# Performance work log

Hardware: AMD Instinct MI355X
Metric: run time of the kernel (lower is better)

The kernel has to match this reference:

```python
import jax, jax.numpy as jnp
import numpy as np

RADIUS = 400.0
FIELD = 8000.0  # um extent of slide coordinate field


def setup_inputs() -> dict:
    key = jax.random.key(0)
    ks = jax.random.split(key, 8)
    B, N, D, H, K = 4, 4096, 1536, 512, 8
    images = jax.random.normal(ks[0], (B, N, D), dtype=jnp.float32)
    positions = jax.random.uniform(ks[1], (B, N, 2), dtype=jnp.float32) * FIELD
    W_feat = jax.random.normal(ks[2], (D, H), dtype=jnp.float32) * (1.0 / np.sqrt(D))
    b_feat = jnp.zeros((H,), dtype=jnp.float32)
    W_pos = jax.random.normal(ks[3], (2, H), dtype=jnp.float32) * 0.5
    W_gnn = jax.random.normal(ks[4], (H, H), dtype=jnp.float32) * (1.0 / np.sqrt(H))
    W_self = jax.random.normal(ks[5], (H, H), dtype=jnp.float32) * (1.0 / np.sqrt(H))
    anchors = jax.random.normal(ks[6], (K, D), dtype=jnp.float32)
    return {"images": images, "positions": positions, "W_feat": W_feat,
            "b_feat": b_feat, "W_pos": W_pos, "W_gnn": W_gnn,
            "W_self": W_self, "anchors": anchors}


def _radius_adjacency(pos):
    # pos: (N, 2). Dense O(N^2) radius graph (mirrors torch.cdist + mask).
    sq = jnp.sum(pos * pos, axis=-1)                       # (N,)
    d2 = sq[:, None] + sq[None, :] - 2.0 * (pos @ pos.T)   # (N, N)
    mask = d2 < (RADIUS * RADIUS)
    N = pos.shape[0]
    mask = mask & ~jnp.eye(N, dtype=bool)                  # no self-loops
    return mask.astype(pos.dtype)


def reference(images, positions, W_feat, b_feat, W_pos, W_gnn, W_self, anchors):
    # --- Stream A: explicit concept quantifier (cosine sim to anchors) ---
    x_norm = images / jnp.clip(jnp.linalg.norm(images, axis=-1, keepdims=True), 1e-12)
    a_norm = anchors / jnp.clip(jnp.linalg.norm(anchors, axis=-1, keepdims=True), 1e-12)
    scores = jnp.einsum('bnd,kd->bnk', x_norm, a_norm)     # (B, N, K)
    concept_profile = scores.mean(axis=1)                  # (B, K)

    # --- Stream B: feature extraction with positional encoding ---
    feat = images @ W_feat + b_feat + positions @ W_pos    # (B, N, H)

    # --- radius graph + one mean-aggregation GNN layer, per slide ---
    def per_graph(f, p):
        A = _radius_adjacency(p)                           # (N, N)
        deg = jnp.clip(A.sum(axis=-1, keepdims=True), 1.0) # (N, 1)
        h = jax.nn.relu(f)
        agg = (A @ h) / deg                                # mean over neighbors
        return jax.nn.relu(agg @ W_gnn + f @ W_self)       # (N, H)

    refined = jax.vmap(per_graph)(feat, positions)         # (B, N, H)
    latent_spatial = refined.mean(axis=1)                  # (B, H)  per-graph mean pool

    return jnp.concatenate([latent_spatial, concept_profile], axis=1)  # (B, H+K)
```

## Files before the change

kernel.cpp:

```cpp
#include <hip/hip_runtime.h>

#define B_ 4
#define N_ 4096
#define D_ 1536
#define H_ 512
#define K_ 8
#define M_ (B_*N_)
#define R2_ 160000.0f
#define CAP 192

typedef __attribute__((ext_vector_type(8))) short bf16x8;
typedef __attribute__((ext_vector_type(4))) float f32x4;

__device__ __forceinline__ unsigned short f2bf(float f) {
  union { float f; unsigned u; } v; v.f = f;
  unsigned r = (v.u + 0x7FFFu + ((v.u >> 16) & 1u)) >> 16;
  return (unsigned short)r;
}

typedef const __attribute__((address_space(1))) unsigned int gas_u32;
typedef __attribute__((address_space(3))) unsigned int las_u32;
__device__ __forceinline__ void gl_lds16(const unsigned short* g, unsigned short* l) {
  __builtin_amdgcn_global_load_lds((gas_u32*)g, (las_u32*)l, 16, 0, 0);
}

__global__ __launch_bounds__(256) void k_prep(
    const float* __restrict__ Wf, const float* __restrict__ Wg, const float* __restrict__ Ws,
    const float* __restrict__ anchors, unsigned short* __restrict__ WfT,
    unsigned short* __restrict__ WgsT, float* __restrict__ anorm) {
  __shared__ float t[64][65];
  __shared__ float red[4];
  int bx = blockIdx.x, by = blockIdx.y, tid = threadIdx.x;
  if (by == 40) {
    int k = bx;
    float s = 0.f;
    for (int i = tid; i < D_; i += 256) { float v = anchors[k*D_ + i]; s += v*v; }
    #pragma unroll
    for (int off = 32; off; off >>= 1) s += __shfl_down(s, off);
    if ((tid & 63) == 0) red[tid >> 6] = s;
    __syncthreads();
    if (tid == 0) anorm[k] = fmaxf(sqrtf(red[0]+red[1]+red[2]+red[3]), 1e-12f);
    return;
  }
  const float* W; unsigned short* WT; int kt, outStride, outOff;
  if (by < 24)      { W = Wf; WT = WfT;  kt = by;      outStride = D_;   outOff = 0; }
  else if (by < 32) { W = Wg; WT = WgsT; kt = by - 24; outStride = 1024; outOff = 0; }
  else              { W = Ws; WT = WgsT; kt = by - 32; outStride = 1024; outOff = 512; }
  int tx = tid & 63, ty = tid >> 6;
  #pragma unroll
  for (int r = 0; r < 64; r += 4)
    t[ty + r][tx] = W[(size_t)(kt*64 + ty + r)*H_ + bx*64 + tx];
  __syncthreads();
  #pragma unroll
  for (int r = 0; r < 64; r += 4) {
    int n = bx*64 + ty + r;
    WT[(size_t)n*outStride + outOff + kt*64 + tx] = f2bf(t[tx][ty + r]);
  }
}

__global__ __launch_bounds__(256) void k_concept_cast(
    const float* __restrict__ images, const float* __restrict__ anchors,
    const float* __restrict__ anorm, unsigned short* __restrict__ imgs_bf,
    float* __restrict__ out) {
  __shared__ float sA[K_*D_];
  __shared__ float sc[4][K_];
  int tid = threadIdx.x, lane = tid & 63, w = tid >> 6;
  {
    const float4* a4 = (const float4*)anchors;
    float4* sA4 = (float4*)sA;
    #pragma unroll
    for (int i = 0; i < 12; i++) sA4[tid + 256*i] = a4[tid + 256*i];
  }
  __syncthreads();
  float acc_k[K_] = {};
  for (int r = 0; r < 8; r++) {
    int gm = blockIdx.x*32 + w*8 + r;
    const float4* xrow = (const float4*)(images + (size_t)gm*D_);
    float nrm = 0.f; float dot[K_] = {};
    #pragma unroll
    for (int it = 0; it < 6; it++) {
      int j = lane + 64*it;
      float4 x = xrow[j];
      nrm += x.x*x.x + x.y*x.y + x.z*x.z + x.w*x.w;
      #pragma unroll
      for (int k = 0; k < K_; k++) {
        float4 a = *(const float4*)&sA[(size_t)(k*384 + j)*4];
        dot[k] += x.x*a.x + x.y*a.y + x.z*a.z + x.w*a.w;
      }
      ushort4 s;
      s.x = f2bf(x.x); s.y = f2bf(x.y); s.z = f2bf(x.z); s.w = f2bf(x.w);
      *(ushort4*)&imgs_bf[(size_t)gm*D_ + (size_t)j*4] = s;
    }
    #pragma unroll
    for (int off = 32; off; off >>= 1) {
      nrm += __shfl_down(nrm, off);
      #pragma unroll
      for (int k = 0; k < K_; k++) dot[k] += __shfl_down(dot[k], off);
    }
    if (lane == 0) {
      float inv = 1.0f / fmaxf(sqrtf(nrm), 1e-12f);
      #pragma unroll
      for (int k = 0; k < K_; k++) acc_k[k] += dot[k] * inv / anorm[k];
    }
  }
  if (lane == 0) {
    #pragma unroll
    for (int k = 0; k < K_; k++) sc[w][k] = acc_k[k];
  }
  __syncthreads();
  if (tid < K_) {
    float s = sc[0][tid] + sc[1][tid] + sc[2][tid] + sc[3][tid];
    int b = blockIdx.x >> 7;
    atomicAdd(out + b*(H_+K_) + H_ + tid, s * (1.0f/N_));
  }
}

#define BM 128
#define BN 128
#define BK 32

__global__ __launch_bounds__(256) void k_gemm(
    const unsigned short* __restrict__ A, const unsigned short* __restrict__ BT,
    int Kdim, int mode, const float* __restrict__ bias, const float* __restrict__ Wpos,
    const float* __restrict__ positions, unsigned short* __restrict__ AB,
    float* __restrict__ out) {
  __shared__ unsigned short As[BM*BK];
  __shared__ unsigned short Bs[BN*BK];
  __shared__ float colsum[BN];
  int tid = threadIdx.x;
  int lane = tid & 63, wv = tid >> 6;
  int wm = wv >> 1, wn = wv & 1;
  int l15 = lane & 15, quad = lane >> 4;
  int bx = blockIdx.x;
  int bm = bx >> 2, bn = bx & 3;
  int m0 = bm*BM, n0 = bn*BN;

  f32x4 acc[4][4] = {};

  int c = wv*2;
  int rowc = (lane >> 2), seg = lane & 3;
  const unsigned short* gA0 = A  + (size_t)(m0 + c*16 + rowc)*Kdim + seg*8;
  const unsigned short* gA1 = gA0 + (size_t)16*Kdim;
  const unsigned short* gB0 = BT + (size_t)(n0 + c*16 + rowc)*Kdim + seg*8;
  const unsigned short* gB1 = gB0 + (size_t)16*Kdim;
  unsigned short* lA0 = As + c*512;
  unsigned short* lA1 = lA0 + 512;
  unsigned short* lB0 = Bs + c*512;
  unsigned short* lB1 = lB0 + 512;

  int nk = Kdim / BK;
  for (int kt = 0; kt < nk; kt++) {
    __syncthreads();
    gl_lds16(gA0, lA0); gl_lds16(gA1, lA1);
    gl_lds16(gB0, lB0); gl_lds16(gB1, lB1);
    gA0 += BK; gA1 += BK; gB0 += BK; gB1 += BK;
    __syncthreads();

    bf16x8 aF[4], bF[4];
    #pragma unroll
    for (int f = 0; f < 4; f++)
      aF[f] = *(const bf16x8*)&As[(wm*64 + f*16 + l15)*BK + quad*8];
    #pragma unroll
    for (int f = 0; f < 4; f++)
      bF[f] = *(const bf16x8*)&Bs[(wn*64 + f*16 + l15)*BK + quad*8];
    #pragma unroll
    for (int mi = 0; mi < 4; mi++)
      #pragma unroll
      for (int ni = 0; ni < 4; ni++)
        acc[mi][ni] = __builtin_amdgcn_mfma_f32_16x16x32_bf16(aF[mi], bF[ni], acc[mi][ni], 0, 0, 0);
  }

  if (mode == 0) {
    float bz[4], w0v[4], w1v[4];
    #pragma unroll
    for (int ni = 0; ni < 4; ni++) {
      int gh = n0 + wn*64 + ni*16 + l15;
      bz[ni] = bias[gh]; w0v[ni] = Wpos[gh]; w1v[ni] = Wpos[H_ + gh];
    }
    #pragma unroll
    for (int mi = 0; mi < 4; mi++) {
      #pragma unroll
      for (int r = 0; r < 4; r++) {
        int gm = m0 + wm*64 + mi*16 + quad*4 + r;
        float2 p = ((const float2*)positions)[gm];
        #pragma unroll
        for (int ni = 0; ni < 4; ni++) {
          int gh = n0 + wn*64 + ni*16 + l15;
          float v = acc[mi][ni][r] + bz[ni] + p.x*w0v[ni] + p.y*w1v[ni];
          AB[(size_t)gm*1024 + 512 + gh] = f2bf(v);
        }
      }
    }
  } else {
    if (tid < BN) colsum[tid] = 0.f;
    __syncthreads();
    #pragma unroll
    for (int ni = 0; ni < 4; ni++) {
      float s = 0.f;
      #pragma unroll
      for (int mi = 0; mi < 4; mi++) {
        #pragma unroll
        for (int r = 0; r < 4; r++) s += fmaxf(acc[mi][ni][r], 0.f);
      }
      s += __shfl_down(s, 32);
      s += __shfl_down(s, 16);
      if (quad == 0) atomicAdd(&colsum[wn*64 + ni*16 + l15], s);
    }
    __syncthreads();
    if (tid < BN) {
      int b = m0 >> 12;
      atomicAdd(out + b*(H_+K_) + n0 + tid, colsum[tid] * (1.0f/N_));
    }
  }
}

__device__ __forceinline__ void acc8(uint4 v, float* a) {
  union { unsigned u; float f; } t;
  t.u = v.x << 16;          a[0] += fmaxf(t.f, 0.f);
  t.u = v.x & 0xFFFF0000u;  a[1] += fmaxf(t.f, 0.f);
  t.u = v.y << 16;          a[2] += fmaxf(t.f, 0.f);
  t.u = v.y & 0xFFFF0000u;  a[3] += fmaxf(t.f, 0.f);
  t.u = v.z << 16;          a[4] += fmaxf(t.f, 0.f);
  t.u = v.z & 0xFFFF0000u;  a[5] += fmaxf(t.f, 0.f);
  t.u = v.w << 16;          a[6] += fmaxf(t.f, 0.f);
  t.u = v.w & 0xFFFF0000u;  a[7] += fmaxf(t.f, 0.f);
}

__global__ __launch_bounds__(256) void k_aggregate(const float* __restrict__ positions,
                                                   unsigned short* __restrict__ AB) {
  __shared__ unsigned short nl[8*CAP];
  __shared__ int cnt[8];
  __shared__ float sdx[8], sdy[8];
  int blk = blockIdx.x;
  int xcd = blk & 7;
  int b = xcd >> 1;
  int sub = ((blk >> 3) << 1) | (xcd & 1);
  int dest0 = sub * 8;
  int tid = threadIdx.x, lane = tid & 63, w = tid >> 6;
  const float2* p2 = (const float2*)(positions + (size_t)b*N_*2);
  if (tid < 8) {
    cnt[tid] = 0;
    float2 pd = p2[dest0 + tid];
    sdx[tid] = pd.x; sdy[tid] = pd.y;
  }
  __syncthreads();
  for (int it = 0; it < 16; it++) {
    int j = tid + 256*it;
    float2 pj = p2[j];
    #pragma unroll
    for (int d = 0; d < 8; d++) {
      float dx = pj.x - sdx[d], dy = pj.y - sdy[d];
      if (dx*dx + dy*dy < R2_ && j != dest0 + d) {
        int p = atomicAdd(&cnt[d], 1);
        if (p < CAP) nl[d*CAP + p] = (unsigned short)j;
      }
    }
  }
  __syncthreads();
  const unsigned short* featb = AB + ((size_t)(b << 12))*1024 + 512 + lane*8;
  #pragma unroll
  for (int dd = 0; dd < 2; dd++) {
    int d = w*2 + dd;
    int deg = cnt[d]; if (deg > CAP) deg = CAP;
    float inv = 1.0f / (float)(deg > 1 ? deg : 1);
    const unsigned short* nlp = &nl[d*CAP];
    float a[8] = {};
    int n = 0;
    for (; n + 4 <= deg; n += 4) {
      ushort4 idx = *(const ushort4*)&nlp[n];
      uint4 v0 = *(const uint4*)(featb + (size_t)idx.x*1024);
      uint4 v1 = *(const uint4*)(featb + (size_t)idx.y*1024);
      uint4 v2 = *(const uint4*)(featb + (size_t)idx.z*1024);
      uint4 v3 = *(const uint4*)(featb + (size_t)idx.w*1024);
      acc8(v0, a); acc8(v1, a); acc8(v2, a); acc8(v3, a);
    }
    for (; n < deg; n++) {
      int j = nlp[n];
      uint4 v = *(const uint4*)(featb + (size_t)j*1024);
      acc8(v, a);
    }
    uint4 o;
    o.x = ((unsigned)f2bf(a[1]*inv) << 16) | f2bf(a[0]*inv);
    o.y = ((unsigned)f2bf(a[3]*inv) << 16) | f2bf(a[2]*inv);
    o.z = ((unsigned)f2bf(a[5]*inv) << 16) | f2bf(a[4]*inv);
    o.w = ((unsigned)f2bf(a[7]*inv) << 16) | f2bf(a[6]*inv);
    *(uint4*)(AB + (size_t)((b << 12) + dest0 + d)*1024 + lane*8) = o;
  }
}

extern "C" void kernel_launch(void* const* d_in, const int* in_sizes, int n_in,
                              void* d_out, int out_size, void* d_ws, size_t ws_size,
                              hipStream_t stream) {
  const float* images    = (const float*)d_in[0];
  const float* positions = (const float*)d_in[1];
  const float* W_feat    = (const float*)d_in[2];
  const float* b_feat    = (const float*)d_in[3];
  const float* W_pos     = (const float*)d_in[4];
  const float* W_gnn     = (const float*)d_in[5];
  const float* W_self    = (const float*)d_in[6];
  const float* anchors   = (const float*)d_in[7];
  float* out = (float*)d_out;

  char* ws = (char*)d_ws;
  unsigned short* imgs_bf = (unsigned short*)ws;
  unsigned short* AB      = (unsigned short*)(ws + 50331648);
  unsigned short* WfT     = (unsigned short*)(ws + 83886080);
  unsigned short* WgsT    = (unsigned short*)(ws + 85458944);
  float*          anorm   = (float*)(ws + 86507520);

  hipMemsetAsync(d_out, 0, sizeof(float)*B_*(H_+K_), stream);
  k_prep<<<dim3(8, 41), 256, 0, stream>>>(W_feat, W_gnn, W_self, anchors, WfT, WgsT, anorm);
  k_concept_cast<<<M_/32, 256, 0, stream>>>(images, anchors, anorm, imgs_bf, out);
  k_gemm<<<512, 256, 0, stream>>>(imgs_bf, WfT, D_, 0, b_feat, W_pos, positions, AB, out);
  k_aggregate<<<2048, 256, 0, stream>>>(positions, AB);
  k_gemm<<<512, 256, 0, stream>>>(AB, WgsT, 1024, 1, nullptr, nullptr, nullptr, AB, out);
}
```

Measured before the change: 310.5 us.

## Quantize relu'd features to fp8 before neighbor aggregation gather

Adds a pass that applies relu to the bf16 features, scales them by 1/64, and packs them to fp8 in a separate buffer that reuses the image workspace. The aggregate kernel then gathers 8-byte fp8 rows instead of 16-byte bf16 rows and folds the scale back into the mean divisor. The aim is to halve the gather traffic in the irregular neighbor aggregation, at the cost of an extra kernel launch with its own read and write of the feature matrix, plus reduced precision in the aggregated features.

```diff
diff --git a/kernel.cpp b/kernel.cpp
--- a/kernel.cpp
+++ b/kernel.cpp
@@ -11,6 +11,7 @@
 
 typedef __attribute__((ext_vector_type(8))) short bf16x8;
 typedef __attribute__((ext_vector_type(4))) float f32x4;
+typedef __attribute__((ext_vector_type(2))) float f32x2;
 
 __device__ __forceinline__ unsigned short f2bf(float f) {
   union { float f; unsigned u; } v; v.f = f;
@@ -214,19 +215,37 @@
   }
 }
 
-__device__ __forceinline__ void acc8(uint4 v, float* a) {
-  union { unsigned u; float f; } t;
-  t.u = v.x << 16;          a[0] += fmaxf(t.f, 0.f);
-  t.u = v.x & 0xFFFF0000u;  a[1] += fmaxf(t.f, 0.f);
-  t.u = v.y << 16;          a[2] += fmaxf(t.f, 0.f);
-  t.u = v.y & 0xFFFF0000u;  a[3] += fmaxf(t.f, 0.f);
-  t.u = v.z << 16;          a[4] += fmaxf(t.f, 0.f);
-  t.u = v.z & 0xFFFF0000u;  a[5] += fmaxf(t.f, 0.f);
-  t.u = v.w << 16;          a[6] += fmaxf(t.f, 0.f);
-  t.u = v.w & 0xFFFF0000u;  a[7] += fmaxf(t.f, 0.f);
+__global__ __launch_bounds__(256) void k_quant(const unsigned short* __restrict__ AB,
+                                               unsigned char* __restrict__ P) {
+  int g = blockIdx.x*256 + threadIdx.x;
+  int row = g >> 6, cg = (g & 63)*8;
+  uint4 v = *(const uint4*)(AB + (size_t)row*1024 + 512 + cg);
+  float f[8];
+  union { unsigned u; float x; } t;
+  t.u = v.x << 16; f[0]=t.x; t.u = v.x & 0xFFFF0000u; f[1]=t.x;
+  t.u = v.y << 16; f[2]=t.x; t.u = v.y & 0xFFFF0000u; f[3]=t.x;
+  t.u = v.z << 16; f[4]=t.x; t.u = v.z & 0xFFFF0000u; f[5]=t.x;
+  t.u = v.w << 16; f[6]=t.x; t.u = v.w & 0xFFFF0000u; f[7]=t.x;
+  #pragma unroll
+  for (int i = 0; i < 8; i++) f[i] = fminf(fmaxf(f[i], 0.f)*0.015625f, 448.f);
+  int u0 = __builtin_amdgcn_cvt_pk_fp8_f32(f[0], f[1], 0, false);
+  u0     = __builtin_amdgcn_cvt_pk_fp8_f32(f[2], f[3], u0, true);
+  int u1 = __builtin_amdgcn_cvt_pk_fp8_f32(f[4], f[5], 0, false);
+  u1     = __builtin_amdgcn_cvt_pk_fp8_f32(f[6], f[7], u1, true);
+  uint2 o; o.x = (unsigned)u0; o.y = (unsigned)u1;
+  *(uint2*)(P + (size_t)row*512 + cg) = o;
+}
+
+__device__ __forceinline__ void accf8(uint2 v, float* a) {
+  f32x2 p;
+  p = __builtin_amdgcn_cvt_pk_f32_fp8(v.x, false); a[0] += p[0]; a[1] += p[1];
+  p = __builtin_amdgcn_cvt_pk_f32_fp8(v.x, true);  a[2] += p[0]; a[3] += p[1];
+  p = __builtin_amdgcn_cvt_pk_f32_fp8(v.y, false); a[4] += p[0]; a[5] += p[1];
+  p = __builtin_amdgcn_cvt_pk_f32_fp8(v.y, true);  a[6] += p[0]; a[7] += p[1];
 }
 
 __global__ __launch_bounds__(256) void k_aggregate(const float* __restrict__ positions,
+                                                   const unsigned char* __restrict__ P,
                                                    unsigned short* __restrict__ AB) {
   __shared__ unsigned short nl[8*CAP];
   __shared__ int cnt[8];
@@ -257,27 +276,27 @@
     }
   }
   __syncthreads();
-  const unsigned short* featb = AB + ((size_t)(b << 12))*1024 + 512 + lane*8;
+  const unsigned char* featb = P + ((size_t)(b << 12))*512 + lane*8;
   #pragma unroll
   for (int dd = 0; dd < 2; dd++) {
     int d = w*2 + dd;
     int deg = cnt[d]; if (deg > CAP) deg = CAP;
-    float inv = 1.0f / (float)(deg > 1 ? deg : 1);
+    float inv = 64.0f / (float)(deg > 1 ? deg : 1);
     const unsigned short* nlp = &nl[d*CAP];
     float a[8] = {};
     int n = 0;
     for (; n + 4 <= deg; n += 4) {
       ushort4 idx = *(const ushort4*)&nlp[n];
-      uint4 v0 = *(const uint4*)(featb + (size_t)idx.x*1024);
-      uint4 v1 = *(const uint4*)(featb + (size_t)idx.y*1024);
-      uint4 v2 = *(const uint4*)(featb + (size_t)idx.z*1024);
-      uint4 v3 = *(const uint4*)(featb + (size_t)idx.w*1024);
-      acc8(v0, a); acc8(v1, a); acc8(v2, a); acc8(v3, a);
+      uint2 v0 = *(const uint2*)(featb + (size_t)idx.x*512);
+      uint2 v1 = *(const uint2*)(featb + (size_t)idx.y*512);
+      uint2 v2 = *(const uint2*)(featb + (size_t)idx.z*512);
+      uint2 v3 = *(const uint2*)(featb + (size_t)idx.w*512);
+      accf8(v0, a); accf8(v1, a); accf8(v2, a); accf8(v3, a);
     }
     for (; n < deg; n++) {
       int j = nlp[n];
-      uint4 v = *(const uint4*)(featb + (size_t)j*1024);
-      acc8(v, a);
+      uint2 v = *(const uint2*)(featb + (size_t)j*512);
+      accf8(v, a);
     }
     uint4 o;
     o.x = ((unsigned)f2bf(a[1]*inv) << 16) | f2bf(a[0]*inv);
@@ -303,6 +322,7 @@
 
   char* ws = (char*)d_ws;
   unsigned short* imgs_bf = (unsigned short*)ws;
+  unsigned char*  P       = (unsigned char*)ws;
   unsigned short* AB      = (unsigned short*)(ws + 50331648);
   unsigned short* WfT     = (unsigned short*)(ws + 83886080);
   unsigned short* WgsT    = (unsigned short*)(ws + 85458944);
@@ -312,6 +332,7 @@
   k_prep<<<dim3(8, 41), 256, 0, stream>>>(W_feat, W_gnn, W_self, anchors, WfT, WgsT, anorm);
   k_concept_cast<<<M_/32, 256, 0, stream>>>(images, anchors, anorm, imgs_bf, out);
   k_gemm<<<512, 256, 0, stream>>>(imgs_bf, WfT, D_, 0, b_feat, W_pos, positions, AB, out);
-  k_aggregate<<<2048, 256, 0, stream>>>(positions, AB);
+  k_quant<<<4096, 256, 0, stream>>>(AB, P);
+  k_aggregate<<<2048, 256, 0, stream>>>(positions, P, AB);
   k_gemm<<<512, 256, 0, stream>>>(AB, WgsT, 1024, 1, nullptr, nullptr, nullptr, AB, out);
 }
```

After: 290.5 us. 6.4% less time.
